# Kernel tuning notes

Hardware: AMD Instinct MI355X
Metric: run time of the kernel (lower is better)

The kernel has to match this reference:

```python
import jax, jax.numpy as jnp
import numpy as np

D_MODEL = 1024
D_STATE = 128
D_CONV = 4
EXPAND = 2
HEADDIM = 64
CHUNK = 64
REWARD_DIM = 1
D_INNER = EXPAND * D_MODEL            # 2048
NHEADS = D_INNER // HEADDIM           # 32
CONV_DIM = D_INNER + D_STATE          # 2176
D_IN_PROJ = 2 * D_INNER + D_STATE + NHEADS  # 4304
B, L = 4, 4096


def _silu(x):
    # NOTE: custom 'silu' in the source: sigmoid(x) + 0.1*x (NOT x*sigmoid(x))
    return jax.nn.sigmoid(x) + 0.1 * x


def _segsum(x):
    """x: (..., T) -> (..., T, T) with out[i,j] = sum_{k=j+1..i} x[k], -inf above diag."""
    T = x.shape[-1]
    lo = jnp.tril(jnp.ones((T, T), bool), -1)
    keep = jnp.tril(jnp.ones((T, T), bool), 0)
    xs = jnp.cumsum(jnp.where(lo, x[..., :, None], 0.0), axis=-2)
    return jnp.where(keep, xs, -jnp.inf)


def _ssd(x, A, B_, C, chunk):
    """x: (b,l,h,p); A: (b,l,h); B_,C: (b,l,n) (shared across heads, head dim 1 in source)."""
    b, l, h, p = x.shape
    t = l // chunk
    x = x.reshape(b, t, chunk, h, p)
    A = A.reshape(b, t, chunk, h).transpose(0, 3, 1, 2)   # b h t l
    B_ = B_.reshape(b, t, chunk, -1)                      # b t l n
    C = C.reshape(b, t, chunk, -1)
    A_cumsum = jnp.cumsum(A, axis=-1)                     # b h t l
    Lm = jnp.exp(_segsum(A))                              # b h t l l
    Y_diag = jnp.einsum('btln,btsn,bhtls,btshp->btlhp', C, B_, Lm, x)
    decay_states = jnp.exp(A_cumsum[..., -1:] - A_cumsum)  # b h t l
    states = jnp.einsum('btln,bhtl,btlhp->bthpn', B_, decay_states, x)
    states = jnp.concatenate([jnp.zeros_like(states[:, :1]), states], axis=1)
    A_last = jnp.pad(A_cumsum[..., -1], ((0, 0), (0, 0), (1, 0)))  # b h (t+1)
    decay_chunk = jnp.exp(_segsum(A_last))                # b h (t+1) (t+1)
    new_states = jnp.einsum('bhzt,bthpn->bzhpn', decay_chunk, states)
    states_prev, final_state = new_states[:, :-1], new_states[:, -1]
    state_decay_out = jnp.exp(A_cumsum)                   # b h t l
    Y_off = jnp.einsum('btln,bthpn,bhtl->btlhp', C, states_prev, state_decay_out)
    Y = (Y_diag + Y_off).reshape(b, l, h, p)
    return Y, final_state


def setup_inputs() -> dict:
    key = jax.random.key(0)
    ks = jax.random.split(key, 12)
    s = 0.02
    return {
        'u': jax.random.normal(ks[0], (B, L, D_MODEL), jnp.float32),
        'reward': jax.random.normal(ks[1], (B, L, REWARD_DIM), jnp.float32),
        'in_w': jax.random.normal(ks[2], (D_IN_PROJ, D_MODEL), jnp.float32) * s,
        'in_b': jax.random.normal(ks[3], (D_IN_PROJ,), jnp.float32) * s,
        'conv_w': jax.random.normal(ks[4], (CONV_DIM, D_CONV), jnp.float32) * 0.2,
        'conv_b': jax.random.normal(ks[5], (CONV_DIM,), jnp.float32) * s,
        'bw': jax.random.normal(ks[6], (D_STATE, REWARD_DIM), jnp.float32) * 0.1,
        'bb': jax.random.normal(ks[7], (D_STATE,), jnp.float32) * 0.1,
        'dt_bias': jax.random.normal(ks[8], (NHEADS,), jnp.float32) * 0.1,
        'A_log': jax.random.normal(ks[9], (NHEADS,), jnp.float32) * 0.1,
        'out_w': jax.random.normal(ks[10], (D_MODEL, D_INNER), jnp.float32) * s,
    }


def reference(u, reward, in_w, in_b, conv_w, conv_b, bw, bb, dt_bias, A_log, out_w):
    b, l, _ = u.shape
    # in_proj + split
    zxcdt = u @ in_w.T + in_b                              # (b,l,4304)
    z = zxcdt[..., :D_INNER]
    xC = zxcdt[..., D_INNER:D_INNER + CONV_DIM]
    dt = jax.nn.softplus(zxcdt[..., D_INNER + CONV_DIM:] + dt_bias)  # (b,l,h)
    # B projection from reward
    B_ = reward @ bw.T + bb                                # (b,l,n)
    # causal depthwise conv (Conv1d pad=d_conv-1, truncated to first l)
    pad = jnp.pad(xC, ((0, 0), (D_CONV - 1, 0), (0, 0)))
    xC_conv = conv_b + sum(pad[:, w:w + l, :] * conv_w[:, w] for w in range(D_CONV))
    xC_conv = _silu(xC_conv)
    x = xC_conv[..., :D_INNER]
    C = jnp.ones((b, l, D_STATE), x.dtype)                 # source overwrites C with ones
    # SSD
    A = -jnp.exp(A_log)                                    # (h,)
    x_heads = x.reshape(b, l, NHEADS, HEADDIM)
    y, ssm_state = _ssd(x_heads * dt[..., None], A * dt, B_, C, CHUNK)
    y = y.reshape(b, l, D_INNER)
    # 'RMSNorm' here is just gating: y * silu(z)
    y = y * _silu(z)
    y = y @ out_w.T
    return y
```

## Files before the change

kernel.cpp:

```cpp
#include <hip/hip_runtime.h>
#include <hip/hip_bf16.h>
#include <math.h>


typedef __attribute__((ext_vector_type(8))) short bf16x8;
typedef __attribute__((ext_vector_type(8))) _Float16 f16x8;
typedef __attribute__((ext_vector_type(4))) float f32x4;

__device__ __forceinline__ float bf2f(unsigned short u) {
    union { float f; unsigned int i; } x; x.i = ((unsigned int)u) << 16; return x.f;
}
__device__ __forceinline__ unsigned short f2bf(float f) {
    union { float f; unsigned int i; } x; x.f = f;
    unsigned int r = x.i + 0x7fffu + ((x.i >> 16) & 1u);
    return (unsigned short)(r >> 16);
}
__device__ __forceinline__ unsigned short f2h(float f) {
    _Float16 h = (_Float16)f;
    unsigned short u; __builtin_memcpy(&u, &h, 2); return u;
}
__device__ __forceinline__ float h2f(unsigned short u) {
    _Float16 h; __builtin_memcpy(&h, &u, 2); return (float)h;
}
__device__ __forceinline__ float softplusf(float x) {
    return (x > 20.f) ? x : log1pf(expf(x));
}
__device__ __forceinline__ float silu_mod(float x) {
    return 1.f / (1.f + expf(-x)) + 0.1f * x;
}
__device__ __forceinline__ void cvt_split2(float x, float y,
                                           unsigned int* hi, unsigned int* lo) {
    __hip_bfloat162 h2 = __float22bfloat162_rn(make_float2(x, y));
    unsigned int h; __builtin_memcpy(&h, &h2, 4);
    union { float f; unsigned int i; } fx, fy;
    fx.i = h << 16;
    fy.i = h & 0xffff0000u;
    __hip_bfloat162 l2 = __float22bfloat162_rn(make_float2(x - fx.f, y - fy.f));
    unsigned int l; __builtin_memcpy(&l, &l2, 4);
    *hi = h; *lo = l;
}
__device__ __forceinline__ void split4(float4 v, ushort4* h, ushort4* l) {
    unsigned short t;
    t = f2bf(v.x); h->x = t; l->x = f2bf(v.x - bf2f(t));
    t = f2bf(v.y); h->y = t; l->y = f2bf(v.y - bf2f(t));
    t = f2bf(v.z); h->z = t; l->z = f2bf(v.z - bf2f(t));
    t = f2bf(v.w); h->w = t; l->w = f2bf(v.w - bf2f(t));
}

template <int KCN_LOG, int REMAP>
__global__ __launch_bounds__(256) void pack_split(
    const float* __restrict__ src, int src_ld,
    unsigned short* __restrict__ h, unsigned short* __restrict__ l)
{
    int t = blockIdx.x * 256 + threadIdx.x;
    int lane = t & 63;
    int kc = (t >> 6) & ((1 << KCN_LOG) - 1);
    int tile = t >> (6 + KCN_LOG);
    int n = tile * 16 + (lane & 15);
    int k = kc * 32 + (lane >> 4) * 8;
    int sr = n;
    if (REMAP) sr = (n < 4096) ? n : (n < 4128 ? n + 128 : -1);
    float4 v0 = make_float4(0.f, 0.f, 0.f, 0.f), v1 = v0;
    if (sr >= 0) {
        const float* s = src + (size_t)sr * src_ld + k;
        v0 = *(const float4*)s;
        v1 = *(const float4*)(s + 4);
    }
    ushort4 h0, l0, h1, l1;
    split4(v0, &h0, &l0);
    split4(v1, &h1, &l1);
    size_t o = (size_t)t * 8;
    *(ushort4*)(h + o) = h0; *(ushort4*)(h + o + 4) = h1;
    *(ushort4*)(l + o) = l0; *(ushort4*)(l + o + 4) = l1;
}

template <int KCN_LOG>
__global__ __launch_bounds__(256) void pack_f16(
    const float* __restrict__ src, unsigned short* __restrict__ d)
{
    int t = blockIdx.x * 256 + threadIdx.x;
    int lane = t & 63;
    int kc = (t >> 6) & ((1 << KCN_LOG) - 1);
    int tile = t >> (6 + KCN_LOG);
    int n = tile * 16 + (lane & 15);
    int k = kc * 32 + (lane >> 4) * 8;
    const float* s = src + (size_t)n * (32 << KCN_LOG) + k;
    float4 v0 = *(const float4*)s;
    float4 v1 = *(const float4*)(s + 4);
    ushort4 h0, h1;
    h0.x = f2h(v0.x); h0.y = f2h(v0.y); h0.z = f2h(v0.z); h0.w = f2h(v0.w);
    h1.x = f2h(v1.x); h1.y = f2h(v1.y); h1.z = f2h(v1.z); h1.w = f2h(v1.w);
    size_t o = (size_t)t * 8;
    *(ushort4*)(d + o) = h0; *(ushort4*)(d + o + 4) = h1;
}

__global__ __launch_bounds__(256) void pack_dtw(
    const float* __restrict__ in_w, float* __restrict__ dtw)
{
    int o = blockIdx.x * 256 + threadIdx.x;
    int k4 = o >> 7, rem = o & 127;
    int h = rem >> 2, r = rem & 3;
    dtw[o] = in_w[(size_t)(4224 + h) * 1024 + k4 * 4 + r];
}

__global__ __launch_bounds__(256) void dtproj2(
    const float* __restrict__ u, const float* __restrict__ dtw,
    const float* __restrict__ in_b, float* __restrict__ dtraw)
{
    int idx = blockIdx.x * 256 + threadIdx.x;
    int l = idx >> 5, h = idx & 31;
    const float* ur = u + (size_t)l * 1024;
    const float* wp = dtw + h * 4;
    float s0 = 0.f, s1 = 0.f, s2 = 0.f, s3 = 0.f;
#pragma unroll 4
    for (int k4 = 0; k4 < 256; k4++) {
        float4 a = *(const float4*)(ur + k4 * 4);
        float4 b = *(const float4*)(wp + (size_t)k4 * 128);
        s0 += a.x * b.x; s1 += a.y * b.y;
        s2 += a.z * b.z; s3 += a.w * b.w;
    }
    dtraw[idx] = (s0 + s1) + (s2 + s3) + in_b[4224 + h];
}

template <int ASRC, int OUT, int KDIM, int KSPLIT, int NOFF>
__global__ __launch_bounds__(256, 2) void mfma_gemm(
    const float* __restrict__ Af,
    const unsigned short* __restrict__ Aph, const unsigned short* __restrict__ Apl,
    const unsigned short* __restrict__ Bph, const unsigned short* __restrict__ Bpl,
    const float* __restrict__ bias,
    float* __restrict__ oz, float* __restrict__ oxc,
    float* __restrict__ dtraw, float* __restrict__ outC)
{
    constexpr int KCN = KDIM / 32;
    constexpr int KCNL = KCN / KSPLIT;
    const int g = blockIdx.x;
    const int ks = (KSPLIT > 1) ? (g >> 8) : 0;
    const int gg = (KSPLIT > 1) ? (g & 255) : g;
    const int m0 = ((gg & 7) * 4 + ((gg >> 3) & 3)) * 128;
    const int n0 = (gg >> 5) * 128 + NOFF;
    const int tid = threadIdx.x;
    const int lane = tid & 63, w = tid >> 6;
    const int wm = w & 1, wn = w >> 1;
    const int fr = lane & 15, q = lane >> 4;
    const size_t koff = (size_t)ks * KCNL * 512;

    const unsigned short* bhp[4];
    const unsigned short* blp[4];
#pragma unroll
    for (int nt = 0; nt < 4; nt++) {
        size_t c = ((size_t)((n0 >> 4) + wn * 4 + nt) * KCN * 64 + lane) * 8 + koff;
        bhp[nt] = Bph + c;
        blp[nt] = Bpl + c;
    }
    const float* afp[4];
    const unsigned short* ahp[4];
    const unsigned short* alp[4];
#pragma unroll
    for (int mt = 0; mt < 4; mt++) {
        if (ASRC == 0) {
            afp[mt] = Af + (size_t)(m0 + wm * 64 + mt * 16 + fr) * KDIM + q * 8
                         + (size_t)ks * (KDIM / KSPLIT);
        } else {
            size_t c = ((size_t)((m0 >> 4) + wm * 4 + mt) * KCN * 64 + lane) * 8 + koff;
            ahp[mt] = Aph + c;
            alp[mt] = Apl + c;
        }
    }

    f32x4 acc[4][4];
#pragma unroll
    for (int i = 0; i < 4; i++)
#pragma unroll
        for (int j = 0; j < 4; j++) acc[i][j] = (f32x4){0.f, 0.f, 0.f, 0.f};

    bf16x8 bh[2][4], bl[2][4], ah[2][4], al[2][4];
    float4 af0[2][4], af1[2][4];

#define LOAD_STEP(B)                                                          \
    {                                                                         \
        _Pragma("unroll") for (int nt = 0; nt < 4; nt++) {                    \
            bh[B][nt] = *(const bf16x8*)bhp[nt];                              \
            bl[B][nt] = *(const bf16x8*)blp[nt];                              \
            bhp[nt] += 512; blp[nt] += 512;                                   \
        }                                                                     \
        _Pragma("unroll") for (int mt = 0; mt < 4; mt++) {                    \
            if (ASRC == 1) {                                                  \
                ah[B][mt] = *(const bf16x8*)ahp[mt];                          \
                al[B][mt] = *(const bf16x8*)alp[mt];                          \
                ahp[mt] += 512; alp[mt] += 512;                               \
            } else {                                                          \
                af0[B][mt] = *(const float4*)afp[mt];                         \
                af1[B][mt] = *(const float4*)(afp[mt] + 4);                   \
                afp[mt] += 32;                                                \
            }                                                                 \
        }                                                                     \
    }

#define MFMA_STEP(B)                                                          \
    {                                                                         \
        bf16x8 xah[4], xal[4];                                                \
        _Pragma("unroll") for (int mt = 0; mt < 4; mt++) {                    \
            if (ASRC == 1) {                                                  \
                xah[mt] = ah[B][mt]; xal[mt] = al[B][mt];                     \
            } else {                                                          \
                union { bf16x8 v; unsigned int u[4]; } H, L;                  \
                cvt_split2(af0[B][mt].x, af0[B][mt].y, &H.u[0], &L.u[0]);     \
                cvt_split2(af0[B][mt].z, af0[B][mt].w, &H.u[1], &L.u[1]);     \
                cvt_split2(af1[B][mt].x, af1[B][mt].y, &H.u[2], &L.u[2]);     \
                cvt_split2(af1[B][mt].z, af1[B][mt].w, &H.u[3], &L.u[3]);     \
                xah[mt] = H.v; xal[mt] = L.v;                                 \
            }                                                                 \
        }                                                                     \
        _Pragma("unroll") for (int mt = 0; mt < 4; mt++)                      \
            _Pragma("unroll") for (int nt = 0; nt < 4; nt++)                  \
                acc[mt][nt] = __builtin_amdgcn_mfma_f32_16x16x32_bf16(        \
                    xah[mt], bh[B][nt], acc[mt][nt], 0, 0, 0);                \
        _Pragma("unroll") for (int mt = 0; mt < 4; mt++)                      \
            _Pragma("unroll") for (int nt = 0; nt < 4; nt++)                  \
                acc[mt][nt] = __builtin_amdgcn_mfma_f32_16x16x32_bf16(        \
                    xah[mt], bl[B][nt], acc[mt][nt], 0, 0, 0);                \
        _Pragma("unroll") for (int mt = 0; mt < 4; mt++)                      \
            _Pragma("unroll") for (int nt = 0; nt < 4; nt++)                  \
                acc[mt][nt] = __builtin_amdgcn_mfma_f32_16x16x32_bf16(        \
                    xal[mt], bh[B][nt], acc[mt][nt], 0, 0, 0);                \
    }

    LOAD_STEP(0);
    for (int kc = 0; kc + 2 < KCNL; kc += 2) {
        LOAD_STEP(1);
        MFMA_STEP(0);
        LOAD_STEP(0);
        MFMA_STEP(1);
    }
    LOAD_STEP(1);
    MFMA_STEP(0);
    MFMA_STEP(1);
#undef LOAD_STEP
#undef MFMA_STEP

#pragma unroll
    for (int nt = 0; nt < 4; nt++) {
        int jn = n0 + wn * 64 + nt * 16 + fr;
        if (OUT == 0 && jn >= 4128) continue;
        float bv = 0.f;
        if (OUT == 0) bv = bias[jn < 4096 ? jn : jn + 128];
#pragma unroll
        for (int mt = 0; mt < 4; mt++) {
#pragma unroll
            for (int reg = 0; reg < 4; reg++) {
                int rm = m0 + wm * 64 + mt * 16 + q * 4 + reg;
                float v = acc[mt][nt][reg] + bv;
                if (OUT == 0) {
                    if (jn < 2048)      oz[(size_t)rm * 2048 + jn] = v;
                    else if (jn < 4096) oxc[(size_t)rm * 2048 + (jn - 2048)] = v;
                    else                dtraw[(size_t)rm * 32 + (jn - 4096)] = v;
                } else {
                    float* dst = (KSPLIT == 1 || ks == 0) ? outC : oz;
                    dst[(size_t)rm * 1024 + jn] = v;
                }
            }
        }
    }
}

template <int KCN, int NT, int OUT>
__global__ __launch_bounds__(512, 4) void gemm256x(
    const unsigned short* __restrict__ Ap, const unsigned short* __restrict__ Bp,
    const float* __restrict__ bias,
    unsigned short* __restrict__ ozh, unsigned short* __restrict__ oxch,
    float* __restrict__ outC)
{
    __shared__ unsigned short smem[24576];
    const int g = blockIdx.x;
    int mb, nb, mbl;
    const unsigned short* Abase = Ap;
    if (OUT == 0) {
        const int xcd = g & 7, loc = g >> 3;
        nb = xcd * 4 + (loc & 3);
        mb = loc >> 2;
        mbl = mb;
    } else {
        nb = g & 7;
        mb = g >> 3;
        mbl = mb & 15;
        Abase = Ap + (size_t)(mb >> 4) * 4096 * 2048;
    }
    const int tid = threadIdx.x;
    const int lane = tid & 63, w = tid >> 6;
    const int wm = w & 3, wn = w >> 2;
    const int fr = lane & 15, q = lane >> 4;

    const unsigned short* gp[3];
    int ldso[3];
#pragma unroll
    for (int i = 0; i < 3; i++) {
        const int c = 3 * w + i;
        if (c < 16) {
            gp[i] = Abase + ((size_t)(mbl * 16 + c) * KCN) * 512 + lane * 8;
            ldso[i] = c * 512;
        } else {
            gp[i] = Bp + ((size_t)(nb * 8 + (c - 16)) * KCN) * 512 + lane * 8;
            ldso[i] = 8192 + (c - 16) * 512;
        }
    }

#define STAGE(BUF)                                                            \
    {                                                                         \
        unsigned short* bp = smem + (BUF) * 12288;                            \
        _Pragma("unroll") for (int i = 0; i < 3; i++) {                       \
            __builtin_amdgcn_global_load_lds(                                 \
                (const __attribute__((address_space(1))) unsigned int*)gp[i], \
                (__attribute__((address_space(3))) unsigned int*)(bp + ldso[i]), \
                16, 0, 0);                                                    \
            gp[i] += 512;                                                     \
        }                                                                     \
    }

    f32x4 acc[4][4];
#pragma unroll
    for (int i = 0; i < 4; i++)
#pragma unroll
        for (int j = 0; j < 4; j++) acc[i][j] = (f32x4){0.f, 0.f, 0.f, 0.f};

    STAGE(0);
    __syncthreads();
    for (int kt = 0; kt < NT; ++kt) {
        const int cur = kt & 1;
        if (kt + 1 < NT) STAGE(cur ^ 1);
        const unsigned short* sb = smem + cur * 12288;
        f16x8 Bv[4];
#pragma unroll
        for (int nt = 0; nt < 4; nt++)
            Bv[nt] = *(const f16x8*)(sb + 8192 + (wn * 4 + nt) * 512 + lane * 8);
#pragma unroll
        for (int mt = 0; mt < 4; mt++) {
            f16x8 av = *(const f16x8*)(sb + (wm * 4 + mt) * 512 + lane * 8);
            __builtin_amdgcn_s_setprio(1);
#pragma unroll
            for (int nt = 0; nt < 4; nt++)
                acc[mt][nt] = __builtin_amdgcn_mfma_f32_16x16x32_f16(
                    av, Bv[nt], acc[mt][nt], 0, 0, 0);
            __builtin_amdgcn_s_setprio(0);
        }
        __syncthreads();
    }
#undef STAGE

    const int m0 = mb * 256, n0 = nb * 128;
#pragma unroll
    for (int nt = 0; nt < 4; nt++) {
        const int jn = n0 + wn * 64 + nt * 16 + fr;
        float bv = 0.f;
        if (OUT == 0) bv = bias[jn];
#pragma unroll
        for (int mt = 0; mt < 4; mt++) {
#pragma unroll
            for (int reg = 0; reg < 4; reg++) {
                const int rm = m0 + wm * 64 + mt * 16 + q * 4 + reg;
                float v = acc[mt][nt][reg] + bv;
                if (OUT == 0) {
                    if (jn < 2048) ozh[(size_t)rm * 2048 + jn] = f2h(v);
                    else           oxch[(size_t)rm * 2048 + (jn - 2048)] = f2h(v);
                } else {
                    outC[(size_t)rm * 1024 + jn] = v;
                }
            }
        }
    }
}

__global__ __launch_bounds__(256) void addOut(
    float* __restrict__ dst, const float* __restrict__ part)
{
    size_t i = ((size_t)blockIdx.x * 256 + threadIdx.x) * 4;
    float4 a = *(const float4*)(dst + i);
    float4 b = *(const float4*)(part + i);
    a.x += b.x; a.y += b.y; a.z += b.z; a.w += b.w;
    *(float4*)(dst + i) = a;
}

template <typename XT, typename YT>
__global__ __launch_bounds__(64) void scanA(
    const XT* __restrict__ xc,
    const float* __restrict__ dtraw, const float* __restrict__ reward,
    const float* __restrict__ conv_w, const float* __restrict__ conv_b,
    const float* __restrict__ dt_bias, const float* __restrict__ A_log,
    const float* __restrict__ bw, const float* __restrict__ bb,
    YT* __restrict__ ylocal,
    float* __restrict__ decay, float* __restrict__ Fb, float* __restrict__ Eb)
{
    const int blk = blockIdx.x;
    const int t = blk & 63;
    const int h = blk >> 6;
    const int p = threadIdx.x;
    const int l0 = t * 64;

    __shared__ float xs[67][65];
    __shared__ float gbuf[64], ebuf[64], dtbuf[64];
    __shared__ float cum63;

    float v1 = bw[p] + bw[p + 64];
    float v2 = bb[p] + bb[p + 64];
#pragma unroll
    for (int o = 32; o > 0; o >>= 1) {
        v1 += __shfl_down(v1, o, 64);
        v2 += __shfl_down(v2, o, 64);
    }
    const float sbw = __shfl(v1, 0, 64);
    const float sbb = __shfl(v2, 0, 64);

    const int l = l0 + p;
    const float dt = softplusf(dtraw[(size_t)l * 32 + h] + dt_bias[h]);
    const float a = -expf(A_log[h]) * dt;
    float cum = a;
#pragma unroll
    for (int o = 1; o < 64; o <<= 1) {
        float uo = __shfl_up(cum, o, 64);
        if (p >= o) cum += uo;
    }
    decay[(size_t)l * 32 + h] = expf(cum);
    gbuf[p] = reward[l] * sbw + sbb;
    ebuf[p] = expf(a);
    dtbuf[p] = dt;
    if (p == 63) cum63 = cum;

    const int c = h * 64 + p;
    for (int r = 0; r < 67; r++) {
        int ls = l0 - 3 + r;
        xs[r][p] = (ls >= 0) ? (float)xc[(size_t)ls * 2048 + c] : 0.f;
    }
    __syncthreads();

    const float w0 = conv_w[c * 4 + 0], w1 = conv_w[c * 4 + 1],
                w2 = conv_w[c * 4 + 2], w3 = conv_w[c * 4 + 3];
    const float cb = conv_b[c];
    float y = 0.f;
    YT* outp = ylocal + (size_t)l0 * 2048 + c;
#pragma unroll 4
    for (int i = 0; i < 64; i++) {
        float v = cb + xs[i][p] * w0 + xs[i + 1][p] * w1 +
                  xs[i + 2][p] * w2 + xs[i + 3][p] * w3;
        float xdt = silu_mod(v) * dtbuf[i];
        y = y * ebuf[i] + gbuf[i] * xdt;
        outp[(size_t)i * 2048] = (YT)y;
    }
    Fb[((size_t)h * 64 + t) * 64 + p] = y;
    if (p == 0) Eb[(size_t)h * 64 + t] = expf(cum63);
}

__global__ __launch_bounds__(64) void scanB(
    const float* __restrict__ Fb, const float* __restrict__ Eb,
    float* __restrict__ Sprev)
{
    int idx = blockIdx.x * blockDim.x + threadIdx.x;
    int p = idx & 63;
    int h = idx >> 6;
    int base = h * 64;
    float S = 0.f;
#pragma unroll 8
    for (int t = 0; t < 64; t++) {
        Sprev[(size_t)(base + t) * 64 + p] = S;
        S = S * Eb[base + t] + Fb[(size_t)(base + t) * 64 + p];
    }
}

__global__ __launch_bounds__(256) void passC(
    const unsigned short* __restrict__ ylh, const unsigned short* __restrict__ zh,
    const float* __restrict__ Sprev, const float* __restrict__ decay,
    unsigned short* __restrict__ ypf)
{
    size_t idx = ((size_t)blockIdx.x * 256 + threadIdx.x) * 4;
    int row = (int)(idx >> 11);
    int cc = (int)(idx & 2047);
    int t = row >> 6;
    int h = cc >> 6, p = cc & 63;
    ushort4 av = *(const ushort4*)(ylh + idx);
    ushort4 zv = *(const ushort4*)(zh + idx);
    float4 sv = *(const float4*)(Sprev + ((size_t)(h * 64 + t)) * 64 + p);
    float d = decay[(size_t)row * 32 + h];
    float4 yv;
    yv.x = (h2f(av.x) + sv.x * d) * silu_mod(h2f(zv.x));
    yv.y = (h2f(av.y) + sv.y * d) * silu_mod(h2f(zv.y));
    yv.z = (h2f(av.z) + sv.z * d) * silu_mod(h2f(zv.z));
    yv.w = (h2f(av.w) + sv.w * d) * silu_mod(h2f(zv.w));
    ushort4 hv;
    hv.x = f2h(yv.x); hv.y = f2h(yv.y); hv.z = f2h(yv.z); hv.w = f2h(yv.w);
    size_t chunk = (((size_t)(row >> 4) * 64 + (cc >> 5)) * 64) + ((cc >> 3) & 3) * 16 + (row & 15);
    size_t o = chunk * 8 + (cc & 7);
    *(ushort4*)(ypf + o) = hv;
}

__global__ __launch_bounds__(256) void passC_bf(
    const float* __restrict__ yl, const float* __restrict__ z,
    const float* __restrict__ Sprev, const float* __restrict__ decay,
    unsigned short* __restrict__ yph, unsigned short* __restrict__ ypl)
{
    size_t idx = ((size_t)blockIdx.x * 256 + threadIdx.x) * 4;
    int row = (int)(idx >> 11);
    int cc = (int)(idx & 2047);
    int t = row >> 6;
    int h = cc >> 6, p = cc & 63;
    float4 av = *(const float4*)(yl + idx);
    float4 bvz = *(const float4*)(z + idx);
    float4 sv = *(const float4*)(Sprev + ((size_t)(h * 64 + t)) * 64 + p);
    float d = decay[(size_t)row * 32 + h];
    float4 yv;
    yv.x = (av.x + sv.x * d) * silu_mod(bvz.x);
    yv.y = (av.y + sv.y * d) * silu_mod(bvz.y);
    yv.z = (av.z + sv.z * d) * silu_mod(bvz.z);
    yv.w = (av.w + sv.w * d) * silu_mod(bvz.w);
    ushort4 hv, lv;
    split4(yv, &hv, &lv);
    size_t chunk = (((size_t)(row >> 4) * 64 + (cc >> 5)) * 64) + ((cc >> 3) & 3) * 16 + (row & 15);
    size_t o = chunk * 8 + (cc & 7);
    *(ushort4*)(yph + o) = hv;
    *(ushort4*)(ypl + o) = lv;
}

extern "C" void kernel_launch(void* const* d_in, const int* in_sizes, int n_in,
                              void* d_out, int out_size, void* d_ws, size_t ws_size,
                              hipStream_t stream)
{
    const float* u       = (const float*)d_in[0];
    const float* reward  = (const float*)d_in[1];
    const float* in_w    = (const float*)d_in[2];
    const float* in_b    = (const float*)d_in[3];
    const float* conv_w  = (const float*)d_in[4];
    const float* conv_b  = (const float*)d_in[5];
    const float* bw      = (const float*)d_in[6];
    const float* bb      = (const float*)d_in[7];
    const float* dt_bias = (const float*)d_in[8];
    const float* A_log   = (const float*)d_in[9];
    const float* out_w   = (const float*)d_in[10];
    float* out = (float*)d_out;

    char* p = (char*)d_ws;
    const size_t SEG = (size_t)4096 * 2048 * 4;
    unsigned short* zh  = (unsigned short*)p;
    unsigned short* xch = (unsigned short*)(p + SEG / 2);
    unsigned short* yp_all = (unsigned short*)(p + SEG);
    float* zf = (float*)p;
    float* xcf = (float*)(p + SEG);
    unsigned short* yph = (unsigned short*)(p + SEG);
    unsigned short* ypl = yph + (size_t)4096 * 2048;
    char* R2 = p + 2 * SEG;
    float* ylocal_f = (float*)R2;
    char* ps = p + 3 * SEG;
    float* dtraw = (float*)ps;                 ps += (size_t)4096 * 32 * 4;
    float* decay = (float*)ps;                 ps += (size_t)4096 * 32 * 4;
    float* Fb    = (float*)ps;                 ps += (size_t)32 * 64 * 64 * 4;
    float* Eb    = (float*)ps;                 ps += (size_t)32 * 64 * 4;
    float* Sprev = (float*)ps;                 ps += (size_t)32 * 64 * 64 * 4;

    const size_t W1PN = (size_t)264 * 32 * 64 * 8;
    const size_t W2PN = (size_t)64 * 64 * 64 * 8;
    const size_t UPN  = (size_t)256 * 32 * 64 * 8;
    const size_t DTWN = 32768;
    size_t used_small = (size_t)(ps - (char*)d_ws);
    bool wonce = ws_size >= used_small + 2 * sizeof(unsigned short) * (W1PN + W2PN);
    bool upack = ws_size >= used_small + 2 * sizeof(unsigned short) * (W1PN + W2PN + UPN)
                           + sizeof(float) * DTWN;

    unsigned short *w1ph, *w1pl, *w2ph, *w2pl;
    unsigned short *uf = nullptr, *w1f = nullptr, *w2f = nullptr;
    unsigned short *ylh = nullptr;
    float* dtw = nullptr;
    if (wonce) {
        w1ph = (unsigned short*)ps;
        w1pl = w1ph + W1PN;
        w2ph = w1pl + W1PN;
        w2pl = w2ph + W2PN;
        if (!upack) {
            pack_split<5, 1><<<2112, 256, 0, stream>>>(in_w, 1024, w1ph, w1pl);
            pack_split<6, 0><<<1024, 256, 0, stream>>>(out_w, 2048, w2ph, w2pl);
        } else {
            w2f = w2ph;
            ylh = w1ph;
            uf  = w2pl + W2PN;
            w1f = uf + UPN;
            dtw = (float*)(w1f + UPN);
            pack_f16<6><<<1024, 256, 0, stream>>>(out_w, w2f);
            pack_f16<5><<<2048, 256, 0, stream>>>(in_w, w1f);
            pack_dtw<<<128, 256, 0, stream>>>(in_w, dtw);
        }
    } else {
        w1ph = (unsigned short*)R2;
        w1pl = w1ph + W1PN;
        w2ph = (unsigned short*)R2;
        w2pl = w2ph + W2PN;
    }

    for (int b = 0; b < 4; b++) {
        const float* ub = u + (size_t)b * 4096 * 1024;
        const float* rb = reward + (size_t)b * 4096;
        float* ob = out + (size_t)b * 4096 * 1024;

        if (!wonce)
            pack_split<5, 1><<<2112, 256, 0, stream>>>(in_w, 1024, w1ph, w1pl);
        if (upack) {
            pack_f16<5><<<2048, 256, 0, stream>>>(ub, uf);
            gemm256x<32, 32, 0><<<512, 512, 0, stream>>>(
                uf, w1f, in_b, zh, xch, nullptr);
            dtproj2<<<512, 256, 0, stream>>>(ub, dtw, in_b, dtraw);
        } else {
            mfma_gemm<0, 0, 1024, 1, 0><<<1056, 256, 0, stream>>>(
                ub, nullptr, nullptr, w1ph, w1pl, in_b, zf, xcf, dtraw, nullptr);
        }
        if (upack) {
            scanA<_Float16, _Float16><<<2048, 64, 0, stream>>>(
                (const _Float16*)xch, dtraw, rb, conv_w, conv_b,
                dt_bias, A_log, bw, bb, (_Float16*)ylh, decay, Fb, Eb);
        } else {
            scanA<float, float><<<2048, 64, 0, stream>>>(
                xcf, dtraw, rb, conv_w, conv_b,
                dt_bias, A_log, bw, bb, ylocal_f, decay, Fb, Eb);
        }
        scanB<<<32, 64, 0, stream>>>(Fb, Eb, Sprev);
        if (upack) {
            passC<<<8192, 256, 0, stream>>>(
                ylh, zh, Sprev, decay, yp_all + (size_t)b * 4096 * 2048);
        } else {
            passC_bf<<<8192, 256, 0, stream>>>(ylocal_f, zf, Sprev, decay, yph, ypl);
        }
        if (!upack) {
            if (!wonce)
                pack_split<6, 0><<<1024, 256, 0, stream>>>(out_w, 2048, w2ph, w2pl);
            mfma_gemm<1, 1, 2048, 2, 0><<<512, 256, 0, stream>>>(
                nullptr, yph, ypl, w2ph, w2pl, nullptr,
                zf, nullptr, nullptr, ob);
            addOut<<<4096, 256, 0, stream>>>(ob, zf);
        }
    }

    if (upack) {
        gemm256x<64, 64, 2><<<512, 512, 0, stream>>>(
            yp_all, w2f, nullptr, nullptr, nullptr, out);
    }
}
```

Measured before the change: 707.7 us.

## Triple-buffer GEMM K-loop with vmcnt waits and batch input packing upfront

The shared GEMM kernel moves from double to triple buffering in LDS. It uses explicit vmcnt waits and raw barriers so two tile loads stay in flight while the current tile is consumed, and the output-GEMM tile-to-block mapping now groups M blocks per XCD. The u-to-f16 packing and dt projection now run once for all batches before the per-batch loop. The packed u is stored in the unused upper half of each batch's yp_all slot, and the raw dt goes to a separate buffer. This removes per-batch small launches and hides load latency, at the cost of more LDS per block, which may lower occupancy.

New measurement: 714.9 us. About the same (+1.0%).

```diff
diff --git a/kernel.cpp b/kernel.cpp
--- a/kernel.cpp
+++ b/kernel.cpp
@@ -91,6 +91,27 @@
     h0.x = f2h(v0.x); h0.y = f2h(v0.y); h0.z = f2h(v0.z); h0.w = f2h(v0.w);
     h1.x = f2h(v1.x); h1.y = f2h(v1.y); h1.z = f2h(v1.z); h1.w = f2h(v1.w);
     size_t o = (size_t)t * 8;
+    *(ushort4*)(d + o) = h0; *(ushort4*)(d + o + 4) = h1;
+}
+
+__global__ __launch_bounds__(256) void pack_f16_all(
+    const float* __restrict__ src, unsigned short* __restrict__ d)
+{
+    int t = blockIdx.x * 256 + threadIdx.x;
+    int b = t >> 19;
+    int tl = t & 0x7ffff;
+    int lane = tl & 63;
+    int kc = (tl >> 6) & 31;
+    int tile = tl >> 11;
+    int n = tile * 16 + (lane & 15);
+    int k = kc * 32 + (lane >> 4) * 8;
+    const float* s = src + (size_t)b * 4096 * 1024 + (size_t)n * 1024 + k;
+    float4 v0 = *(const float4*)s;
+    float4 v1 = *(const float4*)(s + 4);
+    ushort4 h0, h1;
+    h0.x = f2h(v0.x); h0.y = f2h(v0.y); h0.z = f2h(v0.z); h0.w = f2h(v0.w);
+    h1.x = f2h(v1.x); h1.y = f2h(v1.y); h1.z = f2h(v1.z); h1.w = f2h(v1.w);
+    size_t o = (size_t)b * 8388608 + 4194304 + (size_t)tl * 8;
     *(ushort4*)(d + o) = h0; *(ushort4*)(d + o + 4) = h1;
 }
 
@@ -270,7 +291,7 @@
     unsigned short* __restrict__ ozh, unsigned short* __restrict__ oxch,
     float* __restrict__ outC)
 {
-    __shared__ unsigned short smem[24576];
+    __shared__ unsigned short smem[36864];
     const int g = blockIdx.x;
     int mb, nb, mbl;
     const unsigned short* Abase = Ap;
@@ -280,8 +301,9 @@
         mb = loc >> 2;
         mbl = mb;
     } else {
-        nb = g & 7;
-        mb = g >> 3;
+        const int xcd = g & 7, loc = g >> 3;
+        mb = xcd * 8 + (loc & 7);
+        nb = loc >> 3;
         mbl = mb & 15;
         Abase = Ap + (size_t)(mb >> 4) * 4096 * 2048;
     }
@@ -315,6 +337,7 @@
             gp[i] += 512;                                                     \
         }                                                                     \
     }
+#define CFENCE asm volatile("" ::: "memory")
 
     f32x4 acc[4][4];
 #pragma unroll
@@ -323,11 +346,22 @@
         for (int j = 0; j < 4; j++) acc[i][j] = (f32x4){0.f, 0.f, 0.f, 0.f};
 
     STAGE(0);
-    __syncthreads();
+    STAGE(1);
+    int cb = 0;
+    int sbuf = 2;
     for (int kt = 0; kt < NT; ++kt) {
-        const int cur = kt & 1;
-        if (kt + 1 < NT) STAGE(cur ^ 1);
-        const unsigned short* sb = smem + cur * 12288;
+        if (kt + 2 < NT) {
+            STAGE(sbuf);
+            sbuf = (sbuf == 2) ? 0 : sbuf + 1;
+            asm volatile("s_waitcnt vmcnt(6)" ::: "memory");
+        } else if (kt + 1 < NT) {
+            asm volatile("s_waitcnt vmcnt(3)" ::: "memory");
+        } else {
+            asm volatile("s_waitcnt vmcnt(0)" ::: "memory");
+        }
+        __builtin_amdgcn_s_barrier(); CFENCE;
+        const unsigned short* sb = smem + cb * 12288;
+        cb = (cb == 2) ? 0 : cb + 1;
         f16x8 Bv[4];
 #pragma unroll
         for (int nt = 0; nt < 4; nt++)
@@ -342,9 +376,10 @@
                     av, Bv[nt], acc[mt][nt], 0, 0, 0);
             __builtin_amdgcn_s_setprio(0);
         }
-        __syncthreads();
+        __builtin_amdgcn_s_barrier(); CFENCE;
     }
 #undef STAGE
+#undef CFENCE
 
     const int m0 = mb * 256, n0 = nb * 128;
 #pragma unroll
@@ -562,9 +597,10 @@
                            + sizeof(float) * DTWN;
 
     unsigned short *w1ph, *w1pl, *w2ph, *w2pl;
-    unsigned short *uf = nullptr, *w1f = nullptr, *w2f = nullptr;
+    unsigned short *w1f = nullptr, *w2f = nullptr;
     unsigned short *ylh = nullptr;
     float* dtw = nullptr;
+    float* dtraw_all = nullptr;
     if (wonce) {
         w1ph = (unsigned short*)ps;
         w1pl = w1ph + W1PN;
@@ -576,12 +612,15 @@
         } else {
             w2f = w2ph;
             ylh = w1ph;
-            uf  = w2pl + W2PN;
-            w1f = uf + UPN;
+            dtraw_all = (float*)w2pl;
+            unsigned short* uf_slot = w2pl + W2PN;
+            w1f = uf_slot + UPN;
             dtw = (float*)(w1f + UPN);
             pack_f16<6><<<1024, 256, 0, stream>>>(out_w, w2f);
             pack_f16<5><<<2048, 256, 0, stream>>>(in_w, w1f);
             pack_dtw<<<128, 256, 0, stream>>>(in_w, dtw);
+            dtproj2<<<2048, 256, 0, stream>>>(u, dtw, in_b, dtraw_all);
+            pack_f16_all<<<8192, 256, 0, stream>>>(u, yp_all);
         }
     } else {
         w1ph = (unsigned short*)R2;
@@ -598,18 +637,18 @@
         if (!wonce)
             pack_split<5, 1><<<2112, 256, 0, stream>>>(in_w, 1024, w1ph, w1pl);
         if (upack) {
-            pack_f16<5><<<2048, 256, 0, stream>>>(ub, uf);
+            const unsigned short* ufb = yp_all + (size_t)b * 8388608 + 4194304;
             gemm256x<32, 32, 0><<<512, 512, 0, stream>>>(
-                uf, w1f, in_b, zh, xch, nullptr);
-            dtproj2<<<512, 256, 0, stream>>>(ub, dtw, in_b, dtraw);
+                ufb, w1f, in_b, zh, xch, nullptr);
         } else {
             mfma_gemm<0, 0, 1024, 1, 0><<<1056, 256, 0, stream>>>(
                 ub, nullptr, nullptr, w1ph, w1pl, in_b, zf, xcf, dtraw, nullptr);
         }
         if (upack) {
             scanA<_Float16, _Float16><<<2048, 64, 0, stream>>>(
-                (const _Float16*)xch, dtraw, rb, conv_w, conv_b,
-                dt_bias, A_log, bw, bb, (_Float16*)ylh, decay, Fb, Eb);
+                (const _Float16*)xch, dtraw_all + (size_t)b * 4096 * 32,
+                rb, conv_w, conv_b, dt_bias, A_log, bw, bb,
+                (_Float16*)ylh, decay, Fb, Eb);
         } else {
             scanA<float, float><<<2048, 64, 0, stream>>>(
                 xcf, dtraw, rb, conv_w, conv_b,
@@ -618,7 +657,7 @@
         scanB<<<32, 64, 0, stream>>>(Fb, Eb, Sprev);
         if (upack) {
             passC<<<8192, 256, 0, stream>>>(
-                ylh, zh, Sprev, decay, yp_all + (size_t)b * 4096 * 2048);
+                ylh, zh, Sprev, decay, yp_all + (size_t)b * 8388608);
         } else {
             passC_bf<<<8192, 256, 0, stream>>>(ylocal_f, zf, Sprev, decay, yph, ypl);
         }
```
